# Performance work log

Hardware: AMD Instinct MI355X
Metric: run time of the kernel (lower is better)

Reference implementation:

```python
import jax, jax.numpy as jnp
import numpy as np


def setup_inputs() -> dict:
    key = jax.random.key(0)
    k1, k2 = jax.random.split(key)
    n, m, d = 8192, 8192, 64
    x = jax.random.normal(k1, (n, d), dtype=jnp.float32)
    y = jax.random.normal(k2, (m, d), dtype=jnp.float32)
    gamma = jnp.ones((), dtype=jnp.float32)  # learnable bandwidth, init_gamma=1.0
    return {"x": x, "y": y, "gamma": gamma}


def reference(x, y, gamma):
    # RBF kernel: exp(-gamma * ||x_i - y_j||^2), computed via the
    x_sq = jnp.sum(x * x, axis=-1, keepdims=True)          # (n, 1)
    y_sq = jnp.sum(y * y, axis=-1, keepdims=True).T        # (1, m)
    xy = x @ y.T                                           # (n, m) GEMM
    sq_dist = jnp.maximum(x_sq + y_sq - 2.0 * xy, 0.0)     # clamp fp error
    return jnp.exp(-gamma * sq_dist)                       # (n, m)
```

## Files before the change

### kernel.cpp

```cpp
#include <hip/hip_runtime.h>
#include <hip/hip_bf16.h>


#define DD 64
#define BM 128
#define BN 128

typedef __attribute__((ext_vector_type(8))) short short8;
typedef __attribute__((ext_vector_type(4))) float f32x4;

#if __has_builtin(__builtin_amdgcn_exp2f)
#define EXP2(x) __builtin_amdgcn_exp2f(x)
#else
#define EXP2(x) exp2f(x)
#endif

__device__ __forceinline__ unsigned short f2bf_rne(float f) {
  unsigned u = __float_as_uint(f);
  unsigned r = u + 0x7FFFu + ((u >> 16) & 1u);
  return (unsigned short)(r >> 16);
}

__global__ __launch_bounds__(256)
void prep_split(const float* __restrict__ X, const float* __restrict__ Y,
                unsigned short* __restrict__ XHg, unsigned short* __restrict__ XLg,
                unsigned short* __restrict__ YHg, unsigned short* __restrict__ YLg,
                float* __restrict__ xsq, float* __restrict__ ysq, int n) {
  int t = blockIdx.x * 256 + threadIdx.x;
  int row = t >> 4;
  int c4 = t & 15;
  const float* src;
  unsigned short *hd, *ld;
  float* nd;
  int r;
  if (row < n) { r = row;     src = X + (long)r * DD; hd = XHg; ld = XLg; nd = xsq + r; }
  else         { r = row - n; src = Y + (long)r * DD; hd = YHg; ld = YLg; nd = ysq + r; }
  float4 v = ((const float4*)src)[c4];
  float f[4] = {v.x, v.y, v.z, v.w};
  unsigned short h[4], l[4];
#pragma unroll
  for (int q = 0; q < 4; ++q) {
    h[q] = f2bf_rne(f[q]);
    float hv = __uint_as_float(((unsigned)h[q]) << 16);
    l[q] = f2bf_rne(f[q] - hv);
  }
  int sw = (c4 * 8) ^ ((r & 7) << 4);
  *(ushort4*)((char*)hd + (long)r * 128 + sw) = make_ushort4(h[0], h[1], h[2], h[3]);
  *(ushort4*)((char*)ld + (long)r * 128 + sw) = make_ushort4(l[0], l[1], l[2], l[3]);
  float s = v.x * v.x + v.y * v.y + v.z * v.z + v.w * v.w;
  s += __shfl_xor(s, 1);
  s += __shfl_xor(s, 2);
  s += __shfl_xor(s, 4);
  s += __shfl_xor(s, 8);
  if (c4 == 0) *nd = s;
}

__global__ __launch_bounds__(256, 2)
void rbf_mfma_dma(const unsigned short* __restrict__ XHg, const unsigned short* __restrict__ XLg,
                  const unsigned short* __restrict__ YHg, const unsigned short* __restrict__ YLg,
                  const float* __restrict__ gptr,
                  const float* __restrict__ xsq, const float* __restrict__ ysq,
                  float* __restrict__ Out, int mcols) {
  __shared__ __align__(128) char lds[65536];

  const int tid = threadIdx.x;
  const int lane = tid & 63;
  const int wid = tid >> 6;
  const long i0 = (long)blockIdx.y * BM;
  const long j0 = (long)blockIdx.x * BN;

  const char* srcs[4] = {(const char*)XHg + i0 * 128, (const char*)XLg + i0 * 128,
                         (const char*)YHg + j0 * 128, (const char*)YLg + j0 * 128};
#pragma unroll
  for (int t4 = 0; t4 < 4; ++t4) {
#pragma unroll
    for (int it = 0; it < 4; ++it) {
      int off = it * 4096 + wid * 1024;
      const char* g = srcs[t4] + off + lane * 16;
      __builtin_amdgcn_global_load_lds(
          (const __attribute__((address_space(1))) void*)g,
          (__attribute__((address_space(3))) void*)(lds + t4 * 16384 + off),
          16, 0, 0);
    }
  }
  __syncthreads();

  const int wr = wid >> 1, wc = wid & 1;
  const int lr = lane & 15;
  const int hg = lane >> 4;

  f32x4 acc[4][4];
#pragma unroll
  for (int a = 0; a < 4; ++a)
#pragma unroll
    for (int b = 0; b < 4; ++b) acc[a][b] = (f32x4){0.f, 0.f, 0.f, 0.f};

  const char* At[3] = {lds, lds + 16384, lds};
  const char* Bt[3] = {lds + 32768, lds + 32768, lds + 49152};
#pragma unroll
  for (int p = 0; p < 3; ++p) {
#pragma unroll
    for (int s = 0; s < 2; ++s) {
      const int kbyte = s * 64 + hg * 16;
      short8 af[4], bfv[4];
#pragma unroll
      for (int m2 = 0; m2 < 4; ++m2) {
        int row = wr * 64 + m2 * 16 + lr;
        af[m2] = *(const short8*)(At[p] + row * 128 + (kbyte ^ ((row & 7) << 4)));
      }
#pragma unroll
      for (int n2 = 0; n2 < 4; ++n2) {
        int row = wc * 64 + n2 * 16 + lr;
        bfv[n2] = *(const short8*)(Bt[p] + row * 128 + (kbyte ^ ((row & 7) << 4)));
      }
#pragma unroll
      for (int m2 = 0; m2 < 4; ++m2)
#pragma unroll
        for (int n2 = 0; n2 < 4; ++n2)
          acc[m2][n2] = __builtin_amdgcn_mfma_f32_16x16x32_bf16(bfv[n2], af[m2], acc[m2][n2], 0, 0, 0);
    }
  }

  const float g = *gptr;
  const float cf = -g * 1.4426950408889634f;
  const float nc2 = -2.0f * cf;
  float cxr[4];
#pragma unroll
  for (int m2 = 0; m2 < 4; ++m2) cxr[m2] = cf * xsq[i0 + wr * 64 + m2 * 16 + lr];
  float4 cyv[4];
#pragma unroll
  for (int n2 = 0; n2 < 4; ++n2) {
    float4 yq = *(const float4*)&ysq[j0 + wc * 64 + n2 * 16 + hg * 4];
    cyv[n2] = make_float4(cf * yq.x, cf * yq.y, cf * yq.z, cf * yq.w);
  }
#pragma unroll
  for (int m2 = 0; m2 < 4; ++m2) {
    long row = i0 + wr * 64 + m2 * 16 + lr;
    float* op = Out + row * (long)mcols + j0 + wc * 64 + hg * 4;
#pragma unroll
    for (int n2 = 0; n2 < 4; ++n2) {
      float cy[4] = {cyv[n2].x, cyv[n2].y, cyv[n2].z, cyv[n2].w};
      float o[4];
#pragma unroll
      for (int j = 0; j < 4; ++j)
        o[j] = EXP2(fminf(fmaf(nc2, acc[m2][n2][j], cxr[m2] + cy[j]), 0.f));
      *(float4*)(op + n2 * 16) = *(float4*)o;
    }
  }
}

__global__ __launch_bounds__(256)
void prep_sq(const float* __restrict__ X, const float* __restrict__ Y,
             float* __restrict__ xsq, float* __restrict__ ysq, int n) {
  int t = blockIdx.x * 256 + threadIdx.x;
  int row = t >> 4;
  int c = t & 15;
  const float* src;
  float* dst;
  if (row < n) { src = X + (long)row * DD; dst = xsq + row; }
  else         { src = Y + (long)(row - n) * DD; dst = ysq + (row - n); }
  float4 v = ((const float4*)src)[c];
  float s = v.x * v.x + v.y * v.y + v.z * v.z + v.w * v.w;
  s += __shfl_xor(s, 1);
  s += __shfl_xor(s, 2);
  s += __shfl_xor(s, 4);
  s += __shfl_xor(s, 8);
  if (c == 0) *dst = s;
}

__global__ __launch_bounds__(256, 2)
void rbf_mfma_fb(const float* __restrict__ X, const float* __restrict__ Y,
                 const float* __restrict__ gptr,
                 const float* __restrict__ xsq, const float* __restrict__ ysq,
                 float* __restrict__ Out, int mcols) {
  __shared__ unsigned short XH[BM * DD], XL[BM * DD];
  __shared__ unsigned short YH[BN * DD], YL[BN * DD];
  const int tid = threadIdx.x;
  const long i0 = (long)blockIdx.y * BM;
  const long j0 = (long)blockIdx.x * BN;
#pragma unroll
  for (int it = 0; it < 16; ++it) {
    int e = it * 256 + tid;
    int half = e >> 11;
    int idx = e & 2047;
    int row = idx >> 4;
    int c4 = idx & 15;
    const float* src = half ? (Y + (j0 + row) * DD) : (X + (i0 + row) * DD);
    float4 v = ((const float4*)src)[c4];
    float f[4] = {v.x, v.y, v.z, v.w};
    unsigned short h[4], l[4];
#pragma unroll
    for (int q = 0; q < 4; ++q) {
      h[q] = f2bf_rne(f[q]);
      float hv = __uint_as_float(((unsigned)h[q]) << 16);
      l[q] = f2bf_rne(f[q] - hv);
    }
    int sw = (c4 * 8) ^ ((row & 7) << 4);
    unsigned short* Ht = half ? YH : XH;
    unsigned short* Lt = half ? YL : XL;
    *(ushort4*)((char*)Ht + row * 128 + sw) = make_ushort4(h[0], h[1], h[2], h[3]);
    *(ushort4*)((char*)Lt + row * 128 + sw) = make_ushort4(l[0], l[1], l[2], l[3]);
  }
  __syncthreads();
  const int lane = tid & 63;
  const int wid = tid >> 6;
  const int wr = wid >> 1, wc = wid & 1;
  const int lr = lane & 15;
  const int hg = lane >> 4;
  f32x4 acc[4][4];
#pragma unroll
  for (int a = 0; a < 4; ++a)
#pragma unroll
    for (int b = 0; b < 4; ++b) acc[a][b] = (f32x4){0.f, 0.f, 0.f, 0.f};
  const unsigned short* At[3] = {XH, XL, XH};
  const unsigned short* Bt[3] = {YH, YH, YL};
#pragma unroll
  for (int p = 0; p < 3; ++p) {
#pragma unroll
    for (int s = 0; s < 2; ++s) {
      const int kbyte = s * 64 + hg * 16;
      short8 af[4], bfv[4];
#pragma unroll
      for (int m2 = 0; m2 < 4; ++m2) {
        int row = wr * 64 + m2 * 16 + lr;
        af[m2] = *(const short8*)((const char*)At[p] + row * 128 + (kbyte ^ ((row & 7) << 4)));
      }
#pragma unroll
      for (int n2 = 0; n2 < 4; ++n2) {
        int row = wc * 64 + n2 * 16 + lr;
        bfv[n2] = *(const short8*)((const char*)Bt[p] + row * 128 + (kbyte ^ ((row & 7) << 4)));
      }
#pragma unroll
      for (int m2 = 0; m2 < 4; ++m2)
#pragma unroll
        for (int n2 = 0; n2 < 4; ++n2)
          acc[m2][n2] = __builtin_amdgcn_mfma_f32_16x16x32_bf16(af[m2], bfv[n2], acc[m2][n2], 0, 0, 0);
    }
  }
  const float g = *gptr;
  float yv[4];
#pragma unroll
  for (int n2 = 0; n2 < 4; ++n2) yv[n2] = ysq[j0 + wc * 64 + n2 * 16 + lr];
#pragma unroll
  for (int m2 = 0; m2 < 4; ++m2) {
#pragma unroll
    for (int j = 0; j < 4; ++j) {
      long row = i0 + wr * 64 + m2 * 16 + hg * 4 + j;
      float xr = xsq[row];
      float* op = Out + row * (long)mcols + j0 + wc * 64 + lr;
#pragma unroll
      for (int n2 = 0; n2 < 4; ++n2) {
        float d = fmaxf(xr + yv[n2] - 2.0f * acc[m2][n2][j], 0.f);
        op[n2 * 16] = __expf(-g * d);
      }
    }
  }
}

extern "C" void kernel_launch(void* const* d_in, const int* in_sizes, int n_in,
                              void* d_out, int out_size, void* d_ws, size_t ws_size,
                              hipStream_t stream) {
  const float* x = (const float*)d_in[0];
  const float* y = (const float*)d_in[1];
  const float* g = (const float*)d_in[2];
  float* out = (float*)d_out;

  const int n = in_sizes[0] / DD;
  const int m = in_sizes[1] / DD;

  const size_t split_bytes = (size_t)(n + m) * DD * 2 * sizeof(unsigned short);
  const size_t needed = split_bytes + (size_t)(n + m) * sizeof(float);

  dim3 grid(m / BN, n / BM);

  if (ws_size >= needed) {
    unsigned short* XHg = (unsigned short*)d_ws;
    unsigned short* XLg = XHg + (size_t)n * DD;
    unsigned short* YHg = XLg + (size_t)n * DD;
    unsigned short* YLg = YHg + (size_t)m * DD;
    float* xsq = (float*)(YLg + (size_t)m * DD);
    float* ysq = xsq + n;
    prep_split<<<(n + m) / 16, 256, 0, stream>>>(x, y, XHg, XLg, YHg, YLg, xsq, ysq, n);
    rbf_mfma_dma<<<grid, 256, 0, stream>>>(XHg, XLg, YHg, YLg, g, xsq, ysq, out, m);
  } else {
    float* xsq = (float*)d_ws;
    float* ysq = xsq + n;
    prep_sq<<<(n + m) / 16, 256, 0, stream>>>(x, y, xsq, ysq, n);
    rbf_mfma_fb<<<grid, 256, 0, stream>>>(x, y, g, xsq, ysq, out, m);
  }
}
```

Baseline: 60.93 us.

## Make each block loop over eight column tiles, prefetching Y tiles into LDS

Result: slower. 126.8 us (+108.1%).

```diff
diff --git a/kernel.cpp b/kernel.cpp
--- a/kernel.cpp
+++ b/kernel.cpp
@@ -5,6 +5,7 @@
 #define DD 64
 #define BM 128
 #define BN 128
+#define JT 8
 
 typedef __attribute__((ext_vector_type(8))) short short8;
 typedef __attribute__((ext_vector_type(4))) float f32x4;
@@ -56,70 +57,42 @@
 }
 
 __global__ __launch_bounds__(256, 2)
-void rbf_mfma_dma(const unsigned short* __restrict__ XHg, const unsigned short* __restrict__ XLg,
-                  const unsigned short* __restrict__ YHg, const unsigned short* __restrict__ YLg,
-                  const float* __restrict__ gptr,
-                  const float* __restrict__ xsq, const float* __restrict__ ysq,
-                  float* __restrict__ Out, int mcols) {
+void rbf_persist(const unsigned short* __restrict__ XHg, const unsigned short* __restrict__ XLg,
+                 const unsigned short* __restrict__ YHg, const unsigned short* __restrict__ YLg,
+                 const float* __restrict__ gptr,
+                 const float* __restrict__ xsq, const float* __restrict__ ysq,
+                 float* __restrict__ Out, int mcols, int jb) {
   __shared__ __align__(128) char lds[65536];
 
   const int tid = threadIdx.x;
   const int lane = tid & 63;
   const int wid = tid >> 6;
-  const long i0 = (long)blockIdx.y * BM;
-  const long j0 = (long)blockIdx.x * BN;
-
-  const char* srcs[4] = {(const char*)XHg + i0 * 128, (const char*)XLg + i0 * 128,
-                         (const char*)YHg + j0 * 128, (const char*)YLg + j0 * 128};
-#pragma unroll
-  for (int t4 = 0; t4 < 4; ++t4) {
-#pragma unroll
-    for (int it = 0; it < 4; ++it) {
-      int off = it * 4096 + wid * 1024;
-      const char* g = srcs[t4] + off + lane * 16;
-      __builtin_amdgcn_global_load_lds(
-          (const __attribute__((address_space(1))) void*)g,
-          (__attribute__((address_space(3))) void*)(lds + t4 * 16384 + off),
-          16, 0, 0);
-    }
-  }
-  __syncthreads();
+  const int b = blockIdx.x;
+  const int jg = b % jb;
+  const int ip = b / jb;
+  const long i0 = (long)ip * BM;
+
+  {
+    const long jy0 = (long)jg * JT * BN * 128;
+    const char* srcs[4] = {(const char*)XHg + i0 * 128, (const char*)XLg + i0 * 128,
+                           (const char*)YHg + jy0,      (const char*)YLg + jy0};
+#pragma unroll
+    for (int t4 = 0; t4 < 4; ++t4) {
+#pragma unroll
+      for (int it = 0; it < 4; ++it) {
+        int off = it * 4096 + wid * 1024;
+        const char* g = srcs[t4] + off + lane * 16;
+        __builtin_amdgcn_global_load_lds(
+            (const __attribute__((address_space(1))) void*)g,
+            (__attribute__((address_space(3))) void*)(lds + t4 * 16384 + off),
+            16, 0, 0);
+      }
+    }
+  }
 
   const int wr = wid >> 1, wc = wid & 1;
   const int lr = lane & 15;
   const int hg = lane >> 4;
-
-  f32x4 acc[4][4];
-#pragma unroll
-  for (int a = 0; a < 4; ++a)
-#pragma unroll
-    for (int b = 0; b < 4; ++b) acc[a][b] = (f32x4){0.f, 0.f, 0.f, 0.f};
-
-  const char* At[3] = {lds, lds + 16384, lds};
-  const char* Bt[3] = {lds + 32768, lds + 32768, lds + 49152};
-#pragma unroll
-  for (int p = 0; p < 3; ++p) {
-#pragma unroll
-    for (int s = 0; s < 2; ++s) {
-      const int kbyte = s * 64 + hg * 16;
-      short8 af[4], bfv[4];
-#pragma unroll
-      for (int m2 = 0; m2 < 4; ++m2) {
-        int row = wr * 64 + m2 * 16 + lr;
-        af[m2] = *(const short8*)(At[p] + row * 128 + (kbyte ^ ((row & 7) << 4)));
-      }
-#pragma unroll
-      for (int n2 = 0; n2 < 4; ++n2) {
-        int row = wc * 64 + n2 * 16 + lr;
-        bfv[n2] = *(const short8*)(Bt[p] + row * 128 + (kbyte ^ ((row & 7) << 4)));
-      }
-#pragma unroll
-      for (int m2 = 0; m2 < 4; ++m2)
-#pragma unroll
-        for (int n2 = 0; n2 < 4; ++n2)
-          acc[m2][n2] = __builtin_amdgcn_mfma_f32_16x16x32_bf16(bfv[n2], af[m2], acc[m2][n2], 0, 0, 0);
-    }
-  }
 
   const float g = *gptr;
   const float cf = -g * 1.4426950408889634f;
@@ -127,25 +100,89 @@
   float cxr[4];
 #pragma unroll
   for (int m2 = 0; m2 < 4; ++m2) cxr[m2] = cf * xsq[i0 + wr * 64 + m2 * 16 + lr];
-  float4 cyv[4];
-#pragma unroll
-  for (int n2 = 0; n2 < 4; ++n2) {
-    float4 yq = *(const float4*)&ysq[j0 + wc * 64 + n2 * 16 + hg * 4];
-    cyv[n2] = make_float4(cf * yq.x, cf * yq.y, cf * yq.z, cf * yq.w);
-  }
-#pragma unroll
-  for (int m2 = 0; m2 < 4; ++m2) {
-    long row = i0 + wr * 64 + m2 * 16 + lr;
-    float* op = Out + row * (long)mcols + j0 + wc * 64 + hg * 4;
+
+  __syncthreads();
+
+  for (int t = 0; t < JT; ++t) {
+    const long j0 = ((long)jg * JT + t) * BN;
+
+    short8 bf[2][2][4];
+#pragma unroll
+    for (int im = 0; im < 2; ++im)
+#pragma unroll
+      for (int s = 0; s < 2; ++s)
+#pragma unroll
+        for (int n2 = 0; n2 < 4; ++n2) {
+          int row = wc * 64 + n2 * 16 + lr;
+          bf[im][s][n2] = *(const short8*)(lds + 32768 + im * 16384 + row * 128 +
+                                           ((s * 64 + hg * 16) ^ ((row & 7) << 4)));
+        }
+    __syncthreads();
+
+    if (t + 1 < JT) {
+      const char* yh = (const char*)YHg + (j0 + BN) * 128;
+      const char* yl = (const char*)YLg + (j0 + BN) * 128;
+#pragma unroll
+      for (int it = 0; it < 4; ++it) {
+        int off = it * 4096 + wid * 1024;
+        __builtin_amdgcn_global_load_lds(
+            (const __attribute__((address_space(1))) void*)(yh + off + lane * 16),
+            (__attribute__((address_space(3))) void*)(lds + 32768 + off), 16, 0, 0);
+        __builtin_amdgcn_global_load_lds(
+            (const __attribute__((address_space(1))) void*)(yl + off + lane * 16),
+            (__attribute__((address_space(3))) void*)(lds + 49152 + off), 16, 0, 0);
+      }
+    }
+
+    f32x4 acc[4][4];
+#pragma unroll
+    for (int a = 0; a < 4; ++a)
+#pragma unroll
+      for (int c = 0; c < 4; ++c) acc[a][c] = (f32x4){0.f, 0.f, 0.f, 0.f};
+
+    const int AOFF[3] = {0, 16384, 0};
+    const int BIMG[3] = {0, 0, 1};
+#pragma unroll
+    for (int p = 0; p < 3; ++p) {
+#pragma unroll
+      for (int s = 0; s < 2; ++s) {
+        short8 af[4];
+#pragma unroll
+        for (int m2 = 0; m2 < 4; ++m2) {
+          int row = wr * 64 + m2 * 16 + lr;
+          af[m2] = *(const short8*)(lds + AOFF[p] + row * 128 +
+                                    ((s * 64 + hg * 16) ^ ((row & 7) << 4)));
+        }
+#pragma unroll
+        for (int m2 = 0; m2 < 4; ++m2)
+#pragma unroll
+          for (int n2 = 0; n2 < 4; ++n2)
+            acc[m2][n2] = __builtin_amdgcn_mfma_f32_16x16x32_bf16(
+                bf[BIMG[p]][s][n2], af[m2], acc[m2][n2], 0, 0, 0);
+      }
+    }
+
+    float4 cyv[4];
 #pragma unroll
     for (int n2 = 0; n2 < 4; ++n2) {
-      float cy[4] = {cyv[n2].x, cyv[n2].y, cyv[n2].z, cyv[n2].w};
-      float o[4];
-#pragma unroll
-      for (int j = 0; j < 4; ++j)
-        o[j] = EXP2(fminf(fmaf(nc2, acc[m2][n2][j], cxr[m2] + cy[j]), 0.f));
-      *(float4*)(op + n2 * 16) = *(float4*)o;
-    }
+      float4 yq = *(const float4*)&ysq[j0 + wc * 64 + n2 * 16 + hg * 4];
+      cyv[n2] = make_float4(cf * yq.x, cf * yq.y, cf * yq.z, cf * yq.w);
+    }
+#pragma unroll
+    for (int m2 = 0; m2 < 4; ++m2) {
+      long row = i0 + wr * 64 + m2 * 16 + lr;
+      float* op = Out + row * (long)mcols + j0 + wc * 64 + hg * 4;
+#pragma unroll
+      for (int n2 = 0; n2 < 4; ++n2) {
+        float cy[4] = {cyv[n2].x, cyv[n2].y, cyv[n2].z, cyv[n2].w};
+        f32x4 o;
+#pragma unroll
+        for (int j = 0; j < 4; ++j)
+          o[j] = EXP2(fminf(fmaf(nc2, acc[m2][n2][j], cxr[m2] + cy[j]), 0.f));
+        __builtin_nontemporal_store(o, (f32x4*)(op + n2 * 16));
+      }
+    }
+    __syncthreads();
   }
 }
 
@@ -211,7 +248,7 @@
 #pragma unroll
   for (int a = 0; a < 4; ++a)
 #pragma unroll
-    for (int b = 0; b < 4; ++b) acc[a][b] = (f32x4){0.f, 0.f, 0.f, 0.f};
+    for (int c = 0; c < 4; ++c) acc[a][c] = (f32x4){0.f, 0.f, 0.f, 0.f};
   const unsigned short* At[3] = {XH, XL, XH};
   const unsigned short* Bt[3] = {YH, YH, YL};
 #pragma unroll
@@ -271,9 +308,10 @@
   const size_t split_bytes = (size_t)(n + m) * DD * 2 * sizeof(unsigned short);
   const size_t needed = split_bytes + (size_t)(n + m) * sizeof(float);
 
-  dim3 grid(m / BN, n / BM);
-
-  if (ws_size >= needed) {
+  const int nI = n / BM;
+  const int nJ = m / BN;
+
+  if (ws_size >= needed && nJ % JT == 0) {
     unsigned short* XHg = (unsigned short*)d_ws;
     unsigned short* XLg = XHg + (size_t)n * DD;
     unsigned short* YHg = XLg + (size_t)n * DD;
@@ -281,11 +319,13 @@
     float* xsq = (float*)(YLg + (size_t)m * DD);
     float* ysq = xsq + n;
     prep_split<<<(n + m) / 16, 256, 0, stream>>>(x, y, XHg, XLg, YHg, YLg, xsq, ysq, n);
-    rbf_mfma_dma<<<grid, 256, 0, stream>>>(XHg, XLg, YHg, YLg, g, xsq, ysq, out, m);
+    const int jb = nJ / JT;
+    rbf_persist<<<nI * jb, 256, 0, stream>>>(XHg, XLg, YHg, YLg, g, xsq, ysq, out, m, jb);
   } else {
     float* xsq = (float*)d_ws;
     float* ysq = xsq + n;
     prep_sq<<<(n + m) / 16, 256, 0, stream>>>(x, y, xsq, ysq, n);
+    dim3 grid(m / BN, n / BM);
     rbf_mfma_fb<<<grid, 256, 0, stream>>>(x, y, g, xsq, ysq, out, m);
   }
 }
```

## Pre-layout bf16 split operands in MFMA fragment order and drop LDS staging

Applied to the files above, without the earlier changes.

Result: slower. 69.66 us (+14.3%).

```diff
diff --git a/kernel.cpp b/kernel.cpp
--- a/kernel.cpp
+++ b/kernel.cpp
@@ -21,105 +21,110 @@
   return (unsigned short)(r >> 16);
 }
 
+__device__ __forceinline__ long fidx(int p, int s, int rb) {
+  return ((((long)p * 2 + s) * 8) + rb) * 64;
+}
+
 __global__ __launch_bounds__(256)
-void prep_split(const float* __restrict__ X, const float* __restrict__ Y,
-                unsigned short* __restrict__ XHg, unsigned short* __restrict__ XLg,
-                unsigned short* __restrict__ YHg, unsigned short* __restrict__ YLg,
-                float* __restrict__ xsq, float* __restrict__ ysq, int n) {
+void prep_frag(const float* __restrict__ X, const float* __restrict__ Y,
+               short8* __restrict__ XHf, short8* __restrict__ XLf,
+               short8* __restrict__ YHf, short8* __restrict__ YLf,
+               float* __restrict__ xsq, float* __restrict__ ysq, int n) {
   int t = blockIdx.x * 256 + threadIdx.x;
-  int row = t >> 4;
-  int c4 = t & 15;
+  int row_g = t >> 3;
+  int chunk = t & 7;
   const float* src;
-  unsigned short *hd, *ld;
+  short8 *hb, *lb;
   float* nd;
   int r;
-  if (row < n) { r = row;     src = X + (long)r * DD; hd = XHg; ld = XLg; nd = xsq + r; }
-  else         { r = row - n; src = Y + (long)r * DD; hd = YHg; ld = YLg; nd = ysq + r; }
-  float4 v = ((const float4*)src)[c4];
-  float f[4] = {v.x, v.y, v.z, v.w};
-  unsigned short h[4], l[4];
-#pragma unroll
-  for (int q = 0; q < 4; ++q) {
-    h[q] = f2bf_rne(f[q]);
-    float hv = __uint_as_float(((unsigned)h[q]) << 16);
-    l[q] = f2bf_rne(f[q] - hv);
-  }
-  int sw = (c4 * 8) ^ ((r & 7) << 4);
-  *(ushort4*)((char*)hd + (long)r * 128 + sw) = make_ushort4(h[0], h[1], h[2], h[3]);
-  *(ushort4*)((char*)ld + (long)r * 128 + sw) = make_ushort4(l[0], l[1], l[2], l[3]);
-  float s = v.x * v.x + v.y * v.y + v.z * v.z + v.w * v.w;
-  s += __shfl_xor(s, 1);
-  s += __shfl_xor(s, 2);
-  s += __shfl_xor(s, 4);
-  s += __shfl_xor(s, 8);
-  if (c4 == 0) *nd = s;
+  if (row_g < n) { r = row_g;     src = X; hb = XHf; lb = XLf; nd = xsq; }
+  else           { r = row_g - n; src = Y; hb = YHf; lb = YLf; nd = ysq; }
+  const float* p = src + (long)r * DD + chunk * 8;
+  float4 v0 = ((const float4*)p)[0];
+  float4 v1 = ((const float4*)p)[1];
+  float f[8] = {v0.x, v0.y, v0.z, v0.w, v1.x, v1.y, v1.z, v1.w};
+
+  short8 h8, l8;
+  float ss = 0.f;
+#pragma unroll
+  for (int q = 0; q < 8; ++q) {
+    unsigned short h = f2bf_rne(f[q]);
+    float hv = __uint_as_float(((unsigned)h) << 16);
+    h8[q] = (short)h;
+    l8[q] = (short)f2bf_rne(f[q] - hv);
+    ss = fmaf(f[q], f[q], ss);
+  }
+  int pn = r >> 7, rb = (r >> 4) & 7, lr = r & 15;
+  int s = chunk >> 2, hg = chunk & 3;
+  long o = fidx(pn, s, rb) + hg * 16 + lr;
+  hb[o] = h8;
+  lb[o] = l8;
+  ss += __shfl_xor(ss, 1);
+  ss += __shfl_xor(ss, 2);
+  ss += __shfl_xor(ss, 4);
+  if (chunk == 0) nd[r] = ss;
 }
 
 __global__ __launch_bounds__(256, 2)
-void rbf_mfma_dma(const unsigned short* __restrict__ XHg, const unsigned short* __restrict__ XLg,
-                  const unsigned short* __restrict__ YHg, const unsigned short* __restrict__ YLg,
-                  const float* __restrict__ gptr,
-                  const float* __restrict__ xsq, const float* __restrict__ ysq,
-                  float* __restrict__ Out, int mcols) {
-  __shared__ __align__(128) char lds[65536];
-
+void rbf_nolds(const short8* __restrict__ XHf, const short8* __restrict__ XLf,
+               const short8* __restrict__ YHf, const short8* __restrict__ YLf,
+               const float* __restrict__ gptr,
+               const float* __restrict__ xsq, const float* __restrict__ ysq,
+               float* __restrict__ Out, int mcols) {
   const int tid = threadIdx.x;
   const int lane = tid & 63;
   const int wid = tid >> 6;
-  const long i0 = (long)blockIdx.y * BM;
-  const long j0 = (long)blockIdx.x * BN;
-
-  const char* srcs[4] = {(const char*)XHg + i0 * 128, (const char*)XLg + i0 * 128,
-                         (const char*)YHg + j0 * 128, (const char*)YLg + j0 * 128};
-#pragma unroll
-  for (int t4 = 0; t4 < 4; ++t4) {
-#pragma unroll
-    for (int it = 0; it < 4; ++it) {
-      int off = it * 4096 + wid * 1024;
-      const char* g = srcs[t4] + off + lane * 16;
-      __builtin_amdgcn_global_load_lds(
-          (const __attribute__((address_space(1))) void*)g,
-          (__attribute__((address_space(3))) void*)(lds + t4 * 16384 + off),
-          16, 0, 0);
-    }
-  }
-  __syncthreads();
-
   const int wr = wid >> 1, wc = wid & 1;
   const int lr = lane & 15;
   const int hg = lane >> 4;
+  const int ip = blockIdx.y;
+  const int jp = blockIdx.x;
+  const long i0 = (long)ip * BM;
+  const long j0 = (long)jp * BN;
+
+  short8 ah[2][4], bh[2][4], al[2][4], bl[2][4];
+#pragma unroll
+  for (int s = 0; s < 2; ++s)
+#pragma unroll
+    for (int q = 0; q < 4; ++q) {
+      ah[s][q] = XHf[fidx(ip, s, wr * 4 + q) + lane];
+      bh[s][q] = YHf[fidx(jp, s, wc * 4 + q) + lane];
+    }
+#pragma unroll
+  for (int s = 0; s < 2; ++s)
+#pragma unroll
+    for (int q = 0; q < 4; ++q) {
+      al[s][q] = XLf[fidx(ip, s, wr * 4 + q) + lane];
+      bl[s][q] = YLf[fidx(jp, s, wc * 4 + q) + lane];
+    }
 
   f32x4 acc[4][4];
 #pragma unroll
   for (int a = 0; a < 4; ++a)
 #pragma unroll
-    for (int b = 0; b < 4; ++b) acc[a][b] = (f32x4){0.f, 0.f, 0.f, 0.f};
-
-  const char* At[3] = {lds, lds + 16384, lds};
-  const char* Bt[3] = {lds + 32768, lds + 32768, lds + 49152};
-#pragma unroll
-  for (int p = 0; p < 3; ++p) {
-#pragma unroll
-    for (int s = 0; s < 2; ++s) {
-      const int kbyte = s * 64 + hg * 16;
-      short8 af[4], bfv[4];
-#pragma unroll
-      for (int m2 = 0; m2 < 4; ++m2) {
-        int row = wr * 64 + m2 * 16 + lr;
-        af[m2] = *(const short8*)(At[p] + row * 128 + (kbyte ^ ((row & 7) << 4)));
-      }
-#pragma unroll
-      for (int n2 = 0; n2 < 4; ++n2) {
-        int row = wc * 64 + n2 * 16 + lr;
-        bfv[n2] = *(const short8*)(Bt[p] + row * 128 + (kbyte ^ ((row & 7) << 4)));
-      }
-#pragma unroll
-      for (int m2 = 0; m2 < 4; ++m2)
-#pragma unroll
-        for (int n2 = 0; n2 < 4; ++n2)
-          acc[m2][n2] = __builtin_amdgcn_mfma_f32_16x16x32_bf16(bfv[n2], af[m2], acc[m2][n2], 0, 0, 0);
-    }
-  }
+    for (int c = 0; c < 4; ++c) acc[a][c] = (f32x4){0.f, 0.f, 0.f, 0.f};
+
+#pragma unroll
+  for (int s = 0; s < 2; ++s)
+#pragma unroll
+    for (int m2 = 0; m2 < 4; ++m2)
+#pragma unroll
+      for (int n2 = 0; n2 < 4; ++n2)
+        acc[m2][n2] = __builtin_amdgcn_mfma_f32_16x16x32_bf16(bh[s][n2], ah[s][m2], acc[m2][n2], 0, 0, 0);
+#pragma unroll
+  for (int s = 0; s < 2; ++s)
+#pragma unroll
+    for (int m2 = 0; m2 < 4; ++m2)
+#pragma unroll
+      for (int n2 = 0; n2 < 4; ++n2)
+        acc[m2][n2] = __builtin_amdgcn_mfma_f32_16x16x32_bf16(bh[s][n2], al[s][m2], acc[m2][n2], 0, 0, 0);
+#pragma unroll
+  for (int s = 0; s < 2; ++s)
+#pragma unroll
+    for (int m2 = 0; m2 < 4; ++m2)
+#pragma unroll
+      for (int n2 = 0; n2 < 4; ++n2)
+        acc[m2][n2] = __builtin_amdgcn_mfma_f32_16x16x32_bf16(bl[s][n2], ah[s][m2], acc[m2][n2], 0, 0, 0);
 
   const float g = *gptr;
   const float cf = -g * 1.4426950408889634f;
@@ -211,7 +216,7 @@
 #pragma unroll
   for (int a = 0; a < 4; ++a)
 #pragma unroll
-    for (int b = 0; b < 4; ++b) acc[a][b] = (f32x4){0.f, 0.f, 0.f, 0.f};
+    for (int c = 0; c < 4; ++c) acc[a][c] = (f32x4){0.f, 0.f, 0.f, 0.f};
   const unsigned short* At[3] = {XH, XL, XH};
   const unsigned short* Bt[3] = {YH, YH, YL};
 #pragma unroll
@@ -273,15 +278,15 @@
 
   dim3 grid(m / BN, n / BM);
 
-  if (ws_size >= needed) {
-    unsigned short* XHg = (unsigned short*)d_ws;
-    unsigned short* XLg = XHg + (size_t)n * DD;
-    unsigned short* YHg = XLg + (size_t)n * DD;
-    unsigned short* YLg = YHg + (size_t)m * DD;
-    float* xsq = (float*)(YLg + (size_t)m * DD);
+  if (ws_size >= needed && (n % BM) == 0 && (m % BN) == 0) {
+    short8* XHf = (short8*)d_ws;
+    short8* XLf = XHf + (size_t)n * DD / 8;
+    short8* YHf = XLf + (size_t)n * DD / 8;
+    short8* YLf = YHf + (size_t)m * DD / 8;
+    float* xsq = (float*)(YLf + (size_t)m * DD / 8);
     float* ysq = xsq + n;
-    prep_split<<<(n + m) / 16, 256, 0, stream>>>(x, y, XHg, XLg, YHg, YLg, xsq, ysq, n);
-    rbf_mfma_dma<<<grid, 256, 0, stream>>>(XHg, XLg, YHg, YLg, g, xsq, ysq, out, m);
+    prep_frag<<<(n + m) * 8 / 256, 256, 0, stream>>>(x, y, XHf, XLf, YHf, YLf, xsq, ysq, n);
+    rbf_nolds<<<grid, 256, 0, stream>>>(XHf, XLf, YHf, YLf, g, xsq, ysq, out, m);
   } else {
     float* xsq = (float*)d_ws;
     float* ysq = xsq + n;
```

## Restructure main kernel to compute and store one column strip at a time

Applied to the files above, without the earlier changes.

Measured after the change: 58.33 us. 1.04x faster.

```diff
diff --git a/kernel.cpp b/kernel.cpp
--- a/kernel.cpp
+++ b/kernel.cpp
@@ -56,11 +56,11 @@
 }
 
 __global__ __launch_bounds__(256, 2)
-void rbf_mfma_dma(const unsigned short* __restrict__ XHg, const unsigned short* __restrict__ XLg,
-                  const unsigned short* __restrict__ YHg, const unsigned short* __restrict__ YLg,
-                  const float* __restrict__ gptr,
-                  const float* __restrict__ xsq, const float* __restrict__ ysq,
-                  float* __restrict__ Out, int mcols) {
+void rbf_strip(const unsigned short* __restrict__ XHg, const unsigned short* __restrict__ XLg,
+               const unsigned short* __restrict__ YHg, const unsigned short* __restrict__ YLg,
+               const float* __restrict__ gptr,
+               const float* __restrict__ xsq, const float* __restrict__ ysq,
+               float* __restrict__ Out, int mcols) {
   __shared__ __align__(128) char lds[65536];
 
   const int tid = threadIdx.x;
@@ -89,37 +89,16 @@
   const int lr = lane & 15;
   const int hg = lane >> 4;
 
-  f32x4 acc[4][4];
-#pragma unroll
-  for (int a = 0; a < 4; ++a)
-#pragma unroll
-    for (int b = 0; b < 4; ++b) acc[a][b] = (f32x4){0.f, 0.f, 0.f, 0.f};
-
-  const char* At[3] = {lds, lds + 16384, lds};
-  const char* Bt[3] = {lds + 32768, lds + 32768, lds + 49152};
-#pragma unroll
-  for (int p = 0; p < 3; ++p) {
-#pragma unroll
-    for (int s = 0; s < 2; ++s) {
-      const int kbyte = s * 64 + hg * 16;
-      short8 af[4], bfv[4];
-#pragma unroll
-      for (int m2 = 0; m2 < 4; ++m2) {
-        int row = wr * 64 + m2 * 16 + lr;
-        af[m2] = *(const short8*)(At[p] + row * 128 + (kbyte ^ ((row & 7) << 4)));
-      }
-#pragma unroll
-      for (int n2 = 0; n2 < 4; ++n2) {
-        int row = wc * 64 + n2 * 16 + lr;
-        bfv[n2] = *(const short8*)(Bt[p] + row * 128 + (kbyte ^ ((row & 7) << 4)));
-      }
-#pragma unroll
-      for (int m2 = 0; m2 < 4; ++m2)
-#pragma unroll
-        for (int n2 = 0; n2 < 4; ++n2)
-          acc[m2][n2] = __builtin_amdgcn_mfma_f32_16x16x32_bf16(bfv[n2], af[m2], acc[m2][n2], 0, 0, 0);
-    }
-  }
+  short8 afh[2][4], afl[2][4];
+#pragma unroll
+  for (int s = 0; s < 2; ++s)
+#pragma unroll
+    for (int m2 = 0; m2 < 4; ++m2) {
+      int row = wr * 64 + m2 * 16 + lr;
+      int off = (s * 64 + hg * 16) ^ ((row & 7) << 4);
+      afh[s][m2] = *(const short8*)(lds + row * 128 + off);
+      afl[s][m2] = *(const short8*)(lds + 16384 + row * 128 + off);
+    }
 
   const float g = *gptr;
   const float cf = -g * 1.4426950408889634f;
@@ -127,23 +106,45 @@
   float cxr[4];
 #pragma unroll
   for (int m2 = 0; m2 < 4; ++m2) cxr[m2] = cf * xsq[i0 + wr * 64 + m2 * 16 + lr];
-  float4 cyv[4];
+
 #pragma unroll
   for (int n2 = 0; n2 < 4; ++n2) {
+    short8 bfh[2], bfl[2];
+#pragma unroll
+    for (int s = 0; s < 2; ++s) {
+      int row = wc * 64 + n2 * 16 + lr;
+      int off = (s * 64 + hg * 16) ^ ((row & 7) << 4);
+      bfh[s] = *(const short8*)(lds + 32768 + row * 128 + off);
+      bfl[s] = *(const short8*)(lds + 49152 + row * 128 + off);
+    }
+
+    f32x4 acc[4];
+#pragma unroll
+    for (int m2 = 0; m2 < 4; ++m2) acc[m2] = (f32x4){0.f, 0.f, 0.f, 0.f};
+
+#pragma unroll
+    for (int s = 0; s < 2; ++s) {
+#pragma unroll
+      for (int m2 = 0; m2 < 4; ++m2)
+        acc[m2] = __builtin_amdgcn_mfma_f32_16x16x32_bf16(bfh[s], afh[s][m2], acc[m2], 0, 0, 0);
+#pragma unroll
+      for (int m2 = 0; m2 < 4; ++m2)
+        acc[m2] = __builtin_amdgcn_mfma_f32_16x16x32_bf16(bfh[s], afl[s][m2], acc[m2], 0, 0, 0);
+#pragma unroll
+      for (int m2 = 0; m2 < 4; ++m2)
+        acc[m2] = __builtin_amdgcn_mfma_f32_16x16x32_bf16(bfl[s], afh[s][m2], acc[m2], 0, 0, 0);
+    }
+
     float4 yq = *(const float4*)&ysq[j0 + wc * 64 + n2 * 16 + hg * 4];
-    cyv[n2] = make_float4(cf * yq.x, cf * yq.y, cf * yq.z, cf * yq.w);
-  }
-#pragma unroll
-  for (int m2 = 0; m2 < 4; ++m2) {
-    long row = i0 + wr * 64 + m2 * 16 + lr;
-    float* op = Out + row * (long)mcols + j0 + wc * 64 + hg * 4;
-#pragma unroll
-    for (int n2 = 0; n2 < 4; ++n2) {
-      float cy[4] = {cyv[n2].x, cyv[n2].y, cyv[n2].z, cyv[n2].w};
+    float cy[4] = {cf * yq.x, cf * yq.y, cf * yq.z, cf * yq.w};
+#pragma unroll
+    for (int m2 = 0; m2 < 4; ++m2) {
+      long row = i0 + wr * 64 + m2 * 16 + lr;
+      float* op = Out + row * (long)mcols + j0 + wc * 64 + hg * 4;
       float o[4];
 #pragma unroll
       for (int j = 0; j < 4; ++j)
-        o[j] = EXP2(fminf(fmaf(nc2, acc[m2][n2][j], cxr[m2] + cy[j]), 0.f));
+        o[j] = EXP2(fminf(fmaf(nc2, acc[m2][j], cxr[m2] + cy[j]), 0.f));
       *(float4*)(op + n2 * 16) = *(float4*)o;
     }
   }
@@ -173,11 +174,11 @@
                  const float* __restrict__ gptr,
                  const float* __restrict__ xsq, const float* __restrict__ ysq,
                  float* __restrict__ Out, int mcols) {
-  __shared__ unsigned short XH[BM * DD], XL[BM * DD];
-  __shared__ unsigned short YH[BN * DD], YL[BN * DD];
+  __shared__ unsigned short XH[128 * DD], XL[128 * DD];
+  __shared__ unsigned short YH[128 * DD], YL[128 * DD];
   const int tid = threadIdx.x;
-  const long i0 = (long)blockIdx.y * BM;
-  const long j0 = (long)blockIdx.x * BN;
+  const long i0 = (long)blockIdx.y * 128;
+  const long j0 = (long)blockIdx.x * 128;
 #pragma unroll
   for (int it = 0; it < 16; ++it) {
     int e = it * 256 + tid;
@@ -211,7 +212,7 @@
 #pragma unroll
   for (int a = 0; a < 4; ++a)
 #pragma unroll
-    for (int b = 0; b < 4; ++b) acc[a][b] = (f32x4){0.f, 0.f, 0.f, 0.f};
+    for (int c = 0; c < 4; ++c) acc[a][c] = (f32x4){0.f, 0.f, 0.f, 0.f};
   const unsigned short* At[3] = {XH, XL, XH};
   const unsigned short* Bt[3] = {YH, YH, YL};
 #pragma unroll
@@ -271,9 +272,7 @@
   const size_t split_bytes = (size_t)(n + m) * DD * 2 * sizeof(unsigned short);
   const size_t needed = split_bytes + (size_t)(n + m) * sizeof(float);
 
-  dim3 grid(m / BN, n / BM);
-
-  if (ws_size >= needed) {
+  if (ws_size >= needed && (n % BM) == 0 && (m % BN) == 0) {
     unsigned short* XHg = (unsigned short*)d_ws;
     unsigned short* XLg = XHg + (size_t)n * DD;
     unsigned short* YHg = XLg + (size_t)n * DD;
@@ -281,11 +280,13 @@
     float* xsq = (float*)(YLg + (size_t)m * DD);
     float* ysq = xsq + n;
     prep_split<<<(n + m) / 16, 256, 0, stream>>>(x, y, XHg, XLg, YHg, YLg, xsq, ysq, n);
-    rbf_mfma_dma<<<grid, 256, 0, stream>>>(XHg, XLg, YHg, YLg, g, xsq, ysq, out, m);
+    dim3 grid(m / BN, n / BM);
+    rbf_strip<<<grid, 256, 0, stream>>>(XHg, XLg, YHg, YLg, g, xsq, ysq, out, m);
   } else {
     float* xsq = (float*)d_ws;
     float* ysq = xsq + n;
     prep_sq<<<(n + m) / 16, 256, 0, stream>>>(x, y, xsq, ysq, n);
-    rbf_mfma_fb<<<grid, 256, 0, stream>>>(x, y, g, xsq, ysq, out, m);
-  }
-}
+    dim3 grid2(m / 128, n / 128);
+    rbf_mfma_fb<<<grid2, 256, 0, stream>>>(x, y, g, xsq, ysq, out, m);
+  }
+}
```
